# Kernel optimization log

Hardware: AMD Instinct MI355X
Metric: run time of the kernel (lower is better)

Reference implementation:

```python
import jax, jax.numpy as jnp
import numpy as np

H = 64  # hidden_size
B, T1, T2, T3 = 4096, 512, 256, 128


def setup_inputs() -> dict:
    key = jax.random.key(0)
    ks = jax.random.split(key, 18)
    s = 1.0 / np.sqrt(H)  # torch LSTMCell init scale
    def p(k, shape, scale):
        return jax.random.normal(k, shape, dtype=jnp.float32) * scale
    return {
        "x1": p(ks[0], (B, T1), 1.0),
        "x2": p(ks[1], (B, T2), 1.0),
        "x3": p(ks[2], (B, T3), 1.0),
        "W_ih3": p(ks[3], (4 * H, 3), s), "W_hh3": p(ks[4], (4 * H, H), s),
        "b_ih3": p(ks[5], (4 * H,), s), "b_hh3": p(ks[6], (4 * H,), s),
        "W_ih2": p(ks[7], (4 * H, 2), s), "W_hh2": p(ks[8], (4 * H, H), s),
        "b_ih2": p(ks[9], (4 * H,), s), "b_hh2": p(ks[10], (4 * H,), s),
        "W_ih1": p(ks[11], (4 * H, 1), s), "W_hh1": p(ks[12], (4 * H, H), s),
        "b_ih1": p(ks[13], (4 * H,), s), "b_hh1": p(ks[14], (4 * H,), s),
        "W_out": p(ks[15], (1, H), s), "b_out": p(ks[16], (1,), s),
    }


def reference(x1, x2, x3,
              W_ih3, W_hh3, b_ih3, b_hh3,
              W_ih2, W_hh2, b_ih2, b_hh2,
              W_ih1, W_hh1, b_ih1, b_hh1,
              W_out, b_out):
    h = W_hh3.shape[1]
    Bb, t1 = x1.shape
    r2, r3 = t1 // x2.shape[1], t1 // x3.shape[1]
    # Pad input weights to width 3; concat order is [x1, x2, x3] (zeros where absent),
    # so padded-column zeros reproduce the narrower cells exactly.
    Wi = jnp.stack([W_ih3,
                    jnp.pad(W_ih2, ((0, 0), (0, 1))),
                    jnp.pad(W_ih1, ((0, 0), (0, 2)))])  # [3, 4H, 3]
    Wh = jnp.stack([W_hh3, W_hh2, W_hh1])               # [3, 4H, H]
    bs = jnp.stack([b_ih3 + b_hh3, b_ih2 + b_hh2, b_ih1 + b_hh1])  # [3, 4H]
    t = np.arange(t1)
    has2 = (t % r2 == 0)
    has3 = (t % r3 == 0)
    assert not np.any(has3 & ~has2), "ratio2 must divide ratio3 for the concat-order mapping"
    # width 3 -> cell3 (type 0), width 2 -> cell2 (type 1), width 1 -> cell1 (type 2)
    step_type = jnp.asarray(2 - has2.astype(np.int32) - has3.astype(np.int32))
    xs = jnp.zeros((t1, Bb, 3), x1.dtype)
    xs = xs.at[:, :, 0].set(x1.T)
    xs = xs.at[::r2, :, 1].set(x2.T)
    xs = xs.at[::r3, :, 2].set(x3.T)

    def step(carry, inp):
        hx, cx = carry
        x, ty = inp
        g = x @ Wi[ty].T + hx @ Wh[ty].T + bs[ty]  # [B, 4H]
        i, f, gg, o = jnp.split(g, 4, axis=-1)     # torch gate order i,f,g,o
        cx = jax.nn.sigmoid(f) * cx + jax.nn.sigmoid(i) * jnp.tanh(gg)
        hx = jax.nn.sigmoid(o) * jnp.tanh(cx)
        return (hx, cx), None

    z = jnp.zeros((Bb, h), x1.dtype)
    (hx, _), _ = jax.lax.scan(step, (z, z), (xs, step_type))
    return jax.nn.sigmoid(hx @ W_out.T + b_out)  # [B, 1]
```

## Files before the change

### kernel.cpp

```cpp
#include <hip/hip_runtime.h>


typedef __attribute__((ext_vector_type(8))) short short8v;
typedef __attribute__((ext_vector_type(4))) float float4v;
typedef __attribute__((ext_vector_type(2))) float float2v;
typedef __attribute__((ext_vector_type(4))) unsigned int uint4v;
typedef __attribute__((ext_vector_type(2))) unsigned int uint2v;

template <int N> struct IC { static constexpr int value = N; };

#define AST 72
#define XSA 516
#define XSB 129

#if __has_builtin(__builtin_amdgcn_exp2f)
#define EXP2F(x) __builtin_amdgcn_exp2f(x)
#else
#define EXP2F(x) exp2f(x)
#endif
#if __has_builtin(__builtin_amdgcn_rcpf)
#define RCPF(x) __builtin_amdgcn_rcpf(x)
#else
#define RCPF(x) (1.0f / (x))
#endif

#define NL2E -1.4426950408889634f
#define NL2E2 -2.8853900817779268f

__device__ __forceinline__ short f2bf(float f) {
  union { float f; unsigned u; } v; v.f = f;
  unsigned r = v.u + 0x7FFFu + ((v.u >> 16) & 1u);
  return (short)(r >> 16);
}
__device__ __forceinline__ float bf2f(short h) {
  union { float f; unsigned u; } v;
  v.u = ((unsigned)(unsigned short)h) << 16;
  return v.f;
}
__device__ __forceinline__ unsigned cvt_pk_bf16(float lo, float hi) {
  unsigned r;
  asm("v_cvt_pk_bf16_f32 %0, %1, %2" : "=v"(r) : "v"(lo), "v"(hi));
  return r;
}
__device__ __forceinline__ float rcp1p(float y) {
  return RCPF(1.0f + EXP2F(y));
}
__device__ __forceinline__ float fsig(float x) { return rcp1p(x * NL2E); }

__global__ __launch_bounds__(256, 1) void mlstm_kernel(
    const float* __restrict__ x1, const float* __restrict__ x2,
    const float* __restrict__ x3,
    const float* __restrict__ Wi3, const float* __restrict__ Wh3,
    const float* __restrict__ bi3, const float* __restrict__ bh3,
    const float* __restrict__ Wi2, const float* __restrict__ Wh2,
    const float* __restrict__ bi2, const float* __restrict__ bh2,
    const float* __restrict__ Wi1, const float* __restrict__ Wh1,
    const float* __restrict__ bi1, const float* __restrict__ bh1,
    const float* __restrict__ Wout, const float* __restrict__ bout,
    float* __restrict__ out) {
  __shared__ __attribute__((aligned(16))) short Ab0[16 * AST];
  __shared__ __attribute__((aligned(16))) short Ab1[16 * AST];
  __shared__ __attribute__((aligned(16))) unsigned xAf[16 * XSA];
  __shared__ __attribute__((aligned(16))) unsigned xBf[16 * XSB];

  const int tid = threadIdx.x;
  const int w = tid >> 6;
  const int lane = tid & 63;
  const int q = lane >> 4;
  const int c = lane & 15;
  const int R0 = blockIdx.x << 4;

  for (int idx = tid; idx < 16 * 256; idx += 256) {
    int m = idx >> 8, tp = idx & 255;
    float2v v1 = *(const float2v*)(x1 + (size_t)(R0 + m) * 512 + 2 * tp);
    float v2 = x2[(size_t)(R0 + m) * 256 + tp];
    xAf[m * XSA + 2 * tp] = cvt_pk_bf16(v1[0], v2);
    xAf[m * XSA + 2 * tp + 1] = cvt_pk_bf16(v1[1], v2);
  }
  for (int idx = tid; idx < 16 * 128; idx += 256) {
    int m = idx >> 7, tt = idx & 127;
    xBf[m * XSB + tt] = cvt_pk_bf16(x3[(size_t)(R0 + m) * 128 + tt], 0.0f);
  }
  for (int idx = tid; idx < 16 * AST; idx += 256) {
    Ab0[idx] = 0;
    Ab1[idx] = 0;
  }

  short8v whs[3][4][2];
  short8v wix[3][4];
  float4v bias4[3][4];
  {
    const float* WhA[3] = {Wh3, Wh2, Wh1};
    const float* WiA[3] = {Wi3, Wi2, Wi1};
    const float* biA[3] = {bi3, bi2, bi1};
    const float* bhA[3] = {bh3, bh2, bh1};
    const int wdt[3] = {3, 2, 1};
#pragma unroll
    for (int ty = 0; ty < 3; ++ty) {
#pragma unroll
      for (int g = 0; g < 4; ++g) {
        const float sg = (g == 2) ? NL2E2 : NL2E;
        const int n = g * 64 + 16 * w + c;
#pragma unroll
        for (int kf = 0; kf < 2; ++kf) {
          short8v v;
#pragma unroll
          for (int j = 0; j < 8; ++j)
            v[j] = f2bf(sg * WhA[ty][n * 64 + kf * 32 + q * 8 + j]);
          whs[ty][g][kf] = v;
        }
        short8v v2 = {0, 0, 0, 0, 0, 0, 0, 0};
        if (q == 0) {
#pragma unroll
          for (int j = 0; j < 3; ++j)
            if (j < wdt[ty]) v2[j] = f2bf(sg * WiA[ty][n * wdt[ty] + j]);
        }
        wix[ty][g] = v2;
        float4v bv;
#pragma unroll
        for (int r = 0; r < 4; ++r) {
          const int nd = g * 64 + 16 * w + 4 * q + r;
          bv[r] = sg * (biA[ty][nd] + bhA[ty][nd]);
        }
        bias4[ty][g] = bv;
      }
    }
  }

  const int afo = c * AST + q * 8;
  const int hwo = c * AST + 16 * w + 4 * q;
  const int xao = c * XSA;
  const int xbo = c * XSB;

  __syncthreads();

  float cx[4] = {0.f, 0.f, 0.f, 0.f};

  auto stepf = [&](auto tyc, unsigned dS, unsigned dx3, const short* rbuf,
                   short* wbuf) {
    constexpr int TY = decltype(tyc)::value;
    uint4v au = {dS, dx3, 0u, 0u};
    short8v a2 = __builtin_bit_cast(short8v, au);
    short8v a0 = *(const short8v*)(rbuf + afo);
    short8v a1 = *(const short8v*)(rbuf + afo + 32);

    float4v acc[4];
#pragma unroll
    for (int g = 0; g < 4; ++g) {
      float4v z = bias4[TY][g];
      z = __builtin_amdgcn_mfma_f32_16x16x32_bf16(wix[TY][g], a2, z, 0, 0, 0);
      z = __builtin_amdgcn_mfma_f32_16x16x32_bf16(whs[TY][g][0], a0, z, 0, 0, 0);
      z = __builtin_amdgcn_mfma_f32_16x16x32_bf16(whs[TY][g][1], a1, z, 0, 0, 0);
      acc[g] = z;
    }

    float h[4];
#pragma unroll
    for (int r = 0; r < 4; ++r) {
      float e0 = EXP2F(acc[0][r]);
      float e1 = EXP2F(acc[1][r]);
      float e2 = EXP2F(__builtin_fminf(acc[2][r], 60.0f));
      float e3 = EXP2F(acc[3][r]);
      float a = 1.0f + e0, b = 1.0f + e1, g2 = 1.0f + e2;
      float ag = a * g2;
      float Rr = RCPF(ag * b);
      float ncx = (__builtin_fmaf(cx[r], ag, (1.0f - e2) * b)) * Rr;
      cx[r] = ncx;
      float e4 = EXP2F(__builtin_fminf(ncx * NL2E2, 60.0f));
      h[r] = (1.0f - e4) * RCPF((1.0f + e3) * (1.0f + e4));
    }
    uint2v pk;
    pk[0] = cvt_pk_bf16(h[0], h[1]);
    pk[1] = cvt_pk_bf16(h[2], h[3]);
    *(uint2v*)(wbuf + hwo) = pk;
    __syncthreads();
  };

  uint4v xd = *(const uint4v*)(xAf + xao);
  unsigned xw = xBf[xbo];

  for (int t4 = 0; t4 < 512; t4 += 4) {
    stepf(IC<0>{}, xd[0], xw, Ab0, Ab1);
    int tp = (t4 + 4 > 508) ? 508 : (t4 + 4);
    uint4v xdn = *(const uint4v*)(xAf + xao + tp);
    unsigned xwn = xBf[xbo + (tp >> 2)];
    stepf(IC<2>{}, xd[1], xw, Ab1, Ab0);
    stepf(IC<1>{}, xd[2], xw, Ab0, Ab1);
    stepf(IC<2>{}, xd[3], xw, Ab1, Ab0);
    xd = xdn;
    xw = xwn;
  }

  if (tid < 16) {
    float s = bout[0];
    const short* hr = Ab0 + tid * AST;
#pragma unroll
    for (int k = 0; k < 64; ++k)
      s = __builtin_fmaf(bf2f(hr[k]), Wout[k], s);
    out[R0 + tid] = fsig(s);
  }
}

extern "C" void kernel_launch(void* const* d_in, const int* in_sizes, int n_in,
                              void* d_out, int out_size, void* d_ws,
                              size_t ws_size, hipStream_t stream) {
  const float* x1 = (const float*)d_in[0];
  const float* x2 = (const float*)d_in[1];
  const float* x3 = (const float*)d_in[2];
  const float* Wi3 = (const float*)d_in[3];
  const float* Wh3 = (const float*)d_in[4];
  const float* bi3 = (const float*)d_in[5];
  const float* bh3 = (const float*)d_in[6];
  const float* Wi2 = (const float*)d_in[7];
  const float* Wh2 = (const float*)d_in[8];
  const float* bi2 = (const float*)d_in[9];
  const float* bh2 = (const float*)d_in[10];
  const float* Wi1 = (const float*)d_in[11];
  const float* Wh1 = (const float*)d_in[12];
  const float* bi1 = (const float*)d_in[13];
  const float* bh1 = (const float*)d_in[14];
  const float* Wout = (const float*)d_in[15];
  const float* bout = (const float*)d_in[16];
  float* out = (float*)d_out;

  hipLaunchKernelGGL(mlstm_kernel, dim3(256), dim3(256), 0, stream,
                     x1, x2, x3, Wi3, Wh3, bi3, bh3, Wi2, Wh2, bi2, bh2,
                     Wi1, Wh1, bi1, bh1, Wout, bout, out);
}
```

Before: 299.4 us.

## Split LSTM recurrence K-dimension across two wave groups with LDS partial-sum exchange

Doubles the block to 8 waves. Each pair of waves splits the hidden-state reduction into two K halves, trades partial gate sums through shared memory, and each finishes the nonlinearity for half the rows. This shortens the per-wave serial MFMA chain and halves per-wave elementwise work on the latency-bound recurrence. It adds a second block barrier and an LDS round-trip every timestep.

```diff
diff --git a/kernel.cpp b/kernel.cpp
--- a/kernel.cpp
+++ b/kernel.cpp
@@ -5,7 +5,6 @@
 typedef __attribute__((ext_vector_type(4))) float float4v;
 typedef __attribute__((ext_vector_type(2))) float float2v;
 typedef __attribute__((ext_vector_type(4))) unsigned int uint4v;
-typedef __attribute__((ext_vector_type(2))) unsigned int uint2v;
 
 template <int N> struct IC { static constexpr int value = N; };
 
@@ -47,7 +46,7 @@
 }
 __device__ __forceinline__ float fsig(float x) { return rcp1p(x * NL2E); }
 
-__global__ __launch_bounds__(256, 1) void mlstm_kernel(
+__global__ __launch_bounds__(512, 1) void mlstm_kernel(
     const float* __restrict__ x1, const float* __restrict__ x2,
     const float* __restrict__ x3,
     const float* __restrict__ Wi3, const float* __restrict__ Wh3,
@@ -62,31 +61,34 @@
   __shared__ __attribute__((aligned(16))) short Ab1[16 * AST];
   __shared__ __attribute__((aligned(16))) unsigned xAf[16 * XSA];
   __shared__ __attribute__((aligned(16))) unsigned xBf[16 * XSB];
+  __shared__ __attribute__((aligned(16))) float Pex[4][2][4][128];
 
   const int tid = threadIdx.x;
-  const int w = tid >> 6;
+  const int wv = tid >> 6;
+  const int p = wv & 3;
+  const int e = wv >> 2;
   const int lane = tid & 63;
   const int q = lane >> 4;
   const int c = lane & 15;
   const int R0 = blockIdx.x << 4;
 
-  for (int idx = tid; idx < 16 * 256; idx += 256) {
+  for (int idx = tid; idx < 16 * 256; idx += 512) {
     int m = idx >> 8, tp = idx & 255;
     float2v v1 = *(const float2v*)(x1 + (size_t)(R0 + m) * 512 + 2 * tp);
     float v2 = x2[(size_t)(R0 + m) * 256 + tp];
     xAf[m * XSA + 2 * tp] = cvt_pk_bf16(v1[0], v2);
     xAf[m * XSA + 2 * tp + 1] = cvt_pk_bf16(v1[1], v2);
   }
-  for (int idx = tid; idx < 16 * 128; idx += 256) {
+  for (int idx = tid; idx < 16 * 128; idx += 512) {
     int m = idx >> 7, tt = idx & 127;
     xBf[m * XSB + tt] = cvt_pk_bf16(x3[(size_t)(R0 + m) * 128 + tt], 0.0f);
   }
-  for (int idx = tid; idx < 16 * AST; idx += 256) {
+  for (int idx = tid; idx < 16 * AST; idx += 512) {
     Ab0[idx] = 0;
     Ab1[idx] = 0;
   }
 
-  short8v whs[3][4][2];
+  short8v whs[3][4];
   short8v wix[3][4];
   float4v bias4[3][4];
   {
@@ -100,17 +102,14 @@
 #pragma unroll
       for (int g = 0; g < 4; ++g) {
         const float sg = (g == 2) ? NL2E2 : NL2E;
-        const int n = g * 64 + 16 * w + c;
-#pragma unroll
-        for (int kf = 0; kf < 2; ++kf) {
-          short8v v;
-#pragma unroll
-          for (int j = 0; j < 8; ++j)
-            v[j] = f2bf(sg * WhA[ty][n * 64 + kf * 32 + q * 8 + j]);
-          whs[ty][g][kf] = v;
-        }
+        const int n = g * 64 + 16 * p + c;
+        short8v v;
+#pragma unroll
+        for (int j = 0; j < 8; ++j)
+          v[j] = f2bf(sg * WhA[ty][n * 64 + e * 32 + q * 8 + j]);
+        whs[ty][g] = v;
         short8v v2 = {0, 0, 0, 0, 0, 0, 0, 0};
-        if (q == 0) {
+        if (e == 0 && q == 0) {
 #pragma unroll
           for (int j = 0; j < 3; ++j)
             if (j < wdt[ty]) v2[j] = f2bf(sg * WiA[ty][n * wdt[ty] + j]);
@@ -119,7 +118,7 @@
         float4v bv;
 #pragma unroll
         for (int r = 0; r < 4; ++r) {
-          const int nd = g * 64 + 16 * w + 4 * q + r;
+          const int nd = g * 64 + 16 * p + 4 * q + r;
           bv[r] = sg * (biA[ty][nd] + bhA[ty][nd]);
         }
         bias4[ty][g] = bv;
@@ -127,63 +126,109 @@
     }
   }
 
-  const int afo = c * AST + q * 8;
-  const int hwo = c * AST + 16 * w + 4 * q;
+  const int afo = c * AST + q * 8 + e * 32;
+  const int hwo = c * AST + 16 * p + 4 * q + 2 * e;
+  float* pwr = &Pex[p][e][0][2 * lane];
+  const float* prd = &Pex[p][1 - e][0][2 * lane];
   const int xao = c * XSA;
   const int xbo = c * XSB;
 
   __syncthreads();
 
-  float cx[4] = {0.f, 0.f, 0.f, 0.f};
+  float cx0 = 0.f, cx1 = 0.f;
 
   auto stepf = [&](auto tyc, unsigned dS, unsigned dx3, const short* rbuf,
                    short* wbuf) {
     constexpr int TY = decltype(tyc)::value;
-    uint4v au = {dS, dx3, 0u, 0u};
-    short8v a2 = __builtin_bit_cast(short8v, au);
-    short8v a0 = *(const short8v*)(rbuf + afo);
-    short8v a1 = *(const short8v*)(rbuf + afo + 32);
+    short8v ah = *(const short8v*)(rbuf + afo);
 
     float4v acc[4];
-#pragma unroll
-    for (int g = 0; g < 4; ++g) {
-      float4v z = bias4[TY][g];
-      z = __builtin_amdgcn_mfma_f32_16x16x32_bf16(wix[TY][g], a2, z, 0, 0, 0);
-      z = __builtin_amdgcn_mfma_f32_16x16x32_bf16(whs[TY][g][0], a0, z, 0, 0, 0);
-      z = __builtin_amdgcn_mfma_f32_16x16x32_bf16(whs[TY][g][1], a1, z, 0, 0, 0);
-      acc[g] = z;
-    }
-
-    float h[4];
-#pragma unroll
-    for (int r = 0; r < 4; ++r) {
-      float e0 = EXP2F(acc[0][r]);
-      float e1 = EXP2F(acc[1][r]);
-      float e2 = EXP2F(__builtin_fminf(acc[2][r], 60.0f));
-      float e3 = EXP2F(acc[3][r]);
-      float a = 1.0f + e0, b = 1.0f + e1, g2 = 1.0f + e2;
+    if (e == 0) {
+      uint4v au = {dS, dx3, 0u, 0u};
+      short8v a2 = __builtin_bit_cast(short8v, au);
+#pragma unroll
+      for (int g = 0; g < 4; ++g) {
+        float4v z = bias4[TY][g];
+        z = __builtin_amdgcn_mfma_f32_16x16x32_bf16(wix[TY][g], a2, z, 0, 0, 0);
+        z = __builtin_amdgcn_mfma_f32_16x16x32_bf16(whs[TY][g], ah, z, 0, 0, 0);
+        acc[g] = z;
+      }
+    } else {
+      const float4v zz = {0.f, 0.f, 0.f, 0.f};
+#pragma unroll
+      for (int g = 0; g < 4; ++g)
+        acc[g] = __builtin_amdgcn_mfma_f32_16x16x32_bf16(whs[TY][g], ah, zz,
+                                                         0, 0, 0);
+    }
+
+    if (e == 0) {
+#pragma unroll
+      for (int g = 0; g < 4; ++g) {
+        float2v o = {acc[g][2], acc[g][3]};
+        *(float2v*)(pwr + g * 128) = o;
+      }
+    } else {
+#pragma unroll
+      for (int g = 0; g < 4; ++g) {
+        float2v o = {acc[g][0], acc[g][1]};
+        *(float2v*)(pwr + g * 128) = o;
+      }
+    }
+    __syncthreads();
+
+    float G[4][2];
+    if (e == 0) {
+#pragma unroll
+      for (int g = 0; g < 4; ++g) {
+        float2v pg = *(const float2v*)(prd + g * 128);
+        G[g][0] = acc[g][0] + pg[0];
+        G[g][1] = acc[g][1] + pg[1];
+      }
+    } else {
+#pragma unroll
+      for (int g = 0; g < 4; ++g) {
+        float2v pg = *(const float2v*)(prd + g * 128);
+        G[g][0] = acc[g][2] + pg[0];
+        G[g][1] = acc[g][3] + pg[1];
+      }
+    }
+
+    float h2[2];
+#pragma unroll
+    for (int u = 0; u < 2; ++u) {
+      float e0v = EXP2F(G[0][u]);
+      float e1v = EXP2F(G[1][u]);
+      float e2v = EXP2F(__builtin_fminf(G[2][u], 60.0f));
+      float e3v = EXP2F(G[3][u]);
+      float a = 1.0f + e0v, b = 1.0f + e1v, g2 = 1.0f + e2v;
       float ag = a * g2;
       float Rr = RCPF(ag * b);
-      float ncx = (__builtin_fmaf(cx[r], ag, (1.0f - e2) * b)) * Rr;
-      cx[r] = ncx;
-      float e4 = EXP2F(__builtin_fminf(ncx * NL2E2, 60.0f));
-      h[r] = (1.0f - e4) * RCPF((1.0f + e3) * (1.0f + e4));
-    }
-    uint2v pk;
-    pk[0] = cvt_pk_bf16(h[0], h[1]);
-    pk[1] = cvt_pk_bf16(h[2], h[3]);
-    *(uint2v*)(wbuf + hwo) = pk;
+      float cxu = u ? cx1 : cx0;
+      float ncx = __builtin_fmaf(cxu, ag, (1.0f - e2v) * b) * Rr;
+      if (u) cx1 = ncx; else cx0 = ncx;
+      float e4v = EXP2F(__builtin_fminf(ncx * NL2E2, 60.0f));
+      h2[u] = (1.0f - e4v) * RCPF((1.0f + e3v) * (1.0f + e4v));
+    }
+    *(unsigned*)(wbuf + hwo) = cvt_pk_bf16(h2[0], h2[1]);
     __syncthreads();
   };
 
-  uint4v xd = *(const uint4v*)(xAf + xao);
-  unsigned xw = xBf[xbo];
+  uint4v xd = {0u, 0u, 0u, 0u};
+  unsigned xw = 0u;
+  if (e == 0) {
+    xd = *(const uint4v*)(xAf + xao);
+    xw = xBf[xbo];
+  }
 
   for (int t4 = 0; t4 < 512; t4 += 4) {
     stepf(IC<0>{}, xd[0], xw, Ab0, Ab1);
-    int tp = (t4 + 4 > 508) ? 508 : (t4 + 4);
-    uint4v xdn = *(const uint4v*)(xAf + xao + tp);
-    unsigned xwn = xBf[xbo + (tp >> 2)];
+    uint4v xdn = xd;
+    unsigned xwn = xw;
+    if (e == 0) {
+      int tp = (t4 + 4 > 508) ? 508 : (t4 + 4);
+      xdn = *(const uint4v*)(xAf + xao + tp);
+      xwn = xBf[xbo + (tp >> 2)];
+    }
     stepf(IC<2>{}, xd[1], xw, Ab1, Ab0);
     stepf(IC<1>{}, xd[2], xw, Ab0, Ab1);
     stepf(IC<2>{}, xd[3], xw, Ab1, Ab0);
@@ -223,7 +268,7 @@
   const float* bout = (const float*)d_in[16];
   float* out = (float*)d_out;
 
-  hipLaunchKernelGGL(mlstm_kernel, dim3(256), dim3(256), 0, stream,
+  hipLaunchKernelGGL(mlstm_kernel, dim3(256), dim3(512), 0, stream,
                      x1, x2, x3, Wi3, Wh3, bi3, bh3, Wi2, Wh2, bi2, bh2,
                      Wi1, Wh1, bi1, bh1, Wout, bout, out);
 }
```

Measured after the change: 421.9 us. 40.9% more time.

## Precompute next step's input-projection MFMA off the critical path; pair reciprocals

Applied to the files above, without the earlier changes.

Moves the x@Wi+bias MFMA for step t+1 into step t, issued after the recurrent MFMAs, so each step's serial chain has two dependent MFMAs instead of three. The activation math now handles two rows at a time and shares one reciprocal between them (two products instead of two RCPs), which cuts the number of transcendental ops. The exp clamps are lowered to 30 and 36 so the paired products stay finite. In exchange it keeps an extra set of accumulator registers live and adds a few multiplies.

```diff
diff --git a/kernel.cpp b/kernel.cpp
--- a/kernel.cpp
+++ b/kernel.cpp
@@ -136,42 +136,62 @@
 
   float cx[4] = {0.f, 0.f, 0.f, 0.f};
 
-  auto stepf = [&](auto tyc, unsigned dS, unsigned dx3, const short* rbuf,
-                   short* wbuf) {
+  float4v zxA[4], zxB[4];
+
+  auto stepf = [&](auto tyc, auto tync, unsigned dSn, unsigned dx3n,
+                   const short* rbuf, short* wbuf, float4v (&zin)[4],
+                   float4v (&zout)[4]) {
     constexpr int TY = decltype(tyc)::value;
-    uint4v au = {dS, dx3, 0u, 0u};
-    short8v a2 = __builtin_bit_cast(short8v, au);
+    constexpr int TYN = decltype(tync)::value;
     short8v a0 = *(const short8v*)(rbuf + afo);
     short8v a1 = *(const short8v*)(rbuf + afo + 32);
 
     float4v acc[4];
 #pragma unroll
     for (int g = 0; g < 4; ++g) {
-      float4v z = bias4[TY][g];
-      z = __builtin_amdgcn_mfma_f32_16x16x32_bf16(wix[TY][g], a2, z, 0, 0, 0);
-      z = __builtin_amdgcn_mfma_f32_16x16x32_bf16(whs[TY][g][0], a0, z, 0, 0, 0);
-      z = __builtin_amdgcn_mfma_f32_16x16x32_bf16(whs[TY][g][1], a1, z, 0, 0, 0);
-      acc[g] = z;
+      float4v z =
+          __builtin_amdgcn_mfma_f32_16x16x32_bf16(whs[TY][g][0], a0, zin[g], 0, 0, 0);
+      acc[g] =
+          __builtin_amdgcn_mfma_f32_16x16x32_bf16(whs[TY][g][1], a1, z, 0, 0, 0);
     }
 
-    float h[4];
-#pragma unroll
-    for (int r = 0; r < 4; ++r) {
-      float e0 = EXP2F(acc[0][r]);
-      float e1 = EXP2F(acc[1][r]);
-      float e2 = EXP2F(__builtin_fminf(acc[2][r], 60.0f));
-      float e3 = EXP2F(acc[3][r]);
-      float a = 1.0f + e0, b = 1.0f + e1, g2 = 1.0f + e2;
-      float ag = a * g2;
-      float Rr = RCPF(ag * b);
-      float ncx = (__builtin_fmaf(cx[r], ag, (1.0f - e2) * b)) * Rr;
-      cx[r] = ncx;
-      float e4 = EXP2F(__builtin_fminf(ncx * NL2E2, 60.0f));
-      h[r] = (1.0f - e4) * RCPF((1.0f + e3) * (1.0f + e4));
+    uint4v aun = {dSn, dx3n, 0u, 0u};
+    short8v a2n = __builtin_bit_cast(short8v, aun);
+#pragma unroll
+    for (int g = 0; g < 4; ++g)
+      zout[g] = __builtin_amdgcn_mfma_f32_16x16x32_bf16(wix[TYN][g], a2n,
+                                                        bias4[TYN][g], 0, 0, 0);
+
+    float h4[4];
+#pragma unroll
+    for (int pr = 0; pr < 2; ++pr) {
+      const int r0 = 2 * pr, r1 = 2 * pr + 1;
+      float e0a = EXP2F(acc[0][r0]), e0b = EXP2F(acc[0][r1]);
+      float e1a = EXP2F(acc[1][r0]), e1b = EXP2F(acc[1][r1]);
+      float e2a = EXP2F(__builtin_fminf(acc[2][r0], 30.0f));
+      float e2b = EXP2F(__builtin_fminf(acc[2][r1], 30.0f));
+      float aa = 1.0f + e0a, ba = 1.0f + e1a, ga = 1.0f + e2a;
+      float ab_ = 1.0f + e0b, bb = 1.0f + e1b, gb = 1.0f + e2b;
+      float aga = aa * ga, agb = ab_ * gb;
+      float Da = aga * ba, Db = agb * bb;
+      float Rp = RCPF(Da * Db);
+      float Ra = Rp * Db, Rb = Rp * Da;
+      float nca = __builtin_fmaf(cx[r0], aga, (1.0f - e2a) * ba) * Ra;
+      float ncb = __builtin_fmaf(cx[r1], agb, (1.0f - e2b) * bb) * Rb;
+      cx[r0] = nca;
+      cx[r1] = ncb;
+      float e3a = EXP2F(acc[3][r0]), e3b = EXP2F(acc[3][r1]);
+      float e4a = EXP2F(__builtin_fminf(nca * NL2E2, 36.0f));
+      float e4b = EXP2F(__builtin_fminf(ncb * NL2E2, 36.0f));
+      float D2a = (1.0f + e3a) * (1.0f + e4a);
+      float D2b = (1.0f + e3b) * (1.0f + e4b);
+      float R2 = RCPF(D2a * D2b);
+      h4[r0] = (1.0f - e4a) * (R2 * D2b);
+      h4[r1] = (1.0f - e4b) * (R2 * D2a);
     }
     uint2v pk;
-    pk[0] = cvt_pk_bf16(h[0], h[1]);
-    pk[1] = cvt_pk_bf16(h[2], h[3]);
+    pk[0] = cvt_pk_bf16(h4[0], h4[1]);
+    pk[1] = cvt_pk_bf16(h4[2], h4[3]);
     *(uint2v*)(wbuf + hwo) = pk;
     __syncthreads();
   };
@@ -179,14 +199,23 @@
   uint4v xd = *(const uint4v*)(xAf + xao);
   unsigned xw = xBf[xbo];
 
+  {
+    uint4v au = {xd[0], xw, 0u, 0u};
+    short8v a2 = __builtin_bit_cast(short8v, au);
+#pragma unroll
+    for (int g = 0; g < 4; ++g)
+      zxA[g] = __builtin_amdgcn_mfma_f32_16x16x32_bf16(wix[0][g], a2,
+                                                       bias4[0][g], 0, 0, 0);
+  }
+
   for (int t4 = 0; t4 < 512; t4 += 4) {
-    stepf(IC<0>{}, xd[0], xw, Ab0, Ab1);
+    stepf(IC<0>{}, IC<2>{}, xd[1], xw, Ab0, Ab1, zxA, zxB);
     int tp = (t4 + 4 > 508) ? 508 : (t4 + 4);
     uint4v xdn = *(const uint4v*)(xAf + xao + tp);
     unsigned xwn = xBf[xbo + (tp >> 2)];
-    stepf(IC<2>{}, xd[1], xw, Ab1, Ab0);
-    stepf(IC<1>{}, xd[2], xw, Ab0, Ab1);
-    stepf(IC<2>{}, xd[3], xw, Ab1, Ab0);
+    stepf(IC<2>{}, IC<1>{}, xd[2], xw, Ab1, Ab0, zxB, zxA);
+    stepf(IC<1>{}, IC<2>{}, xd[3], xw, Ab0, Ab1, zxA, zxB);
+    stepf(IC<2>{}, IC<0>{}, xdn[0], xwn, Ab1, Ab0, zxB, zxA);
     xd = xdn;
     xw = xwn;
   }
```

After: 306.3 us. 1.02x slower.

## Duplicate MFMA per wave pair and split gate activations across 512 threads

Applied to the files above, without the earlier changes.

Doubles the block to 512 threads. Each pair of waves computes the same MFMA gate products redundantly, and each wave then evaluates the activations for only half of the four accumulator rows. Bias is added after the MFMA instead of being seeded into the accumulator. The aim is to halve the serial transcendental work per step on the recurrent critical path. In exchange it doubles MFMA issue, makes the per-step barrier cover 8 waves, adds register pressure under launch_bounds(512,2), and introduces a divergent e==0 branch.

```diff
diff --git a/kernel.cpp b/kernel.cpp
--- a/kernel.cpp
+++ b/kernel.cpp
@@ -5,7 +5,6 @@
 typedef __attribute__((ext_vector_type(4))) float float4v;
 typedef __attribute__((ext_vector_type(2))) float float2v;
 typedef __attribute__((ext_vector_type(4))) unsigned int uint4v;
-typedef __attribute__((ext_vector_type(2))) unsigned int uint2v;
 
 template <int N> struct IC { static constexpr int value = N; };
 
@@ -47,7 +46,7 @@
 }
 __device__ __forceinline__ float fsig(float x) { return rcp1p(x * NL2E); }
 
-__global__ __launch_bounds__(256, 1) void mlstm_kernel(
+__global__ __launch_bounds__(512, 2) void mlstm_kernel(
     const float* __restrict__ x1, const float* __restrict__ x2,
     const float* __restrict__ x3,
     const float* __restrict__ Wi3, const float* __restrict__ Wh3,
@@ -64,31 +63,32 @@
   __shared__ __attribute__((aligned(16))) unsigned xBf[16 * XSB];
 
   const int tid = threadIdx.x;
-  const int w = tid >> 6;
+  const int w = (tid >> 6) & 3;
+  const int e = tid >> 8;
   const int lane = tid & 63;
   const int q = lane >> 4;
   const int c = lane & 15;
   const int R0 = blockIdx.x << 4;
 
-  for (int idx = tid; idx < 16 * 256; idx += 256) {
+  for (int idx = tid; idx < 16 * 256; idx += 512) {
     int m = idx >> 8, tp = idx & 255;
     float2v v1 = *(const float2v*)(x1 + (size_t)(R0 + m) * 512 + 2 * tp);
     float v2 = x2[(size_t)(R0 + m) * 256 + tp];
     xAf[m * XSA + 2 * tp] = cvt_pk_bf16(v1[0], v2);
     xAf[m * XSA + 2 * tp + 1] = cvt_pk_bf16(v1[1], v2);
   }
-  for (int idx = tid; idx < 16 * 128; idx += 256) {
+  for (int idx = tid; idx < 16 * 128; idx += 512) {
     int m = idx >> 7, tt = idx & 127;
     xBf[m * XSB + tt] = cvt_pk_bf16(x3[(size_t)(R0 + m) * 128 + tt], 0.0f);
   }
-  for (int idx = tid; idx < 16 * AST; idx += 256) {
+  for (int idx = tid; idx < 16 * AST; idx += 512) {
     Ab0[idx] = 0;
     Ab1[idx] = 0;
   }
 
   short8v whs[3][4][2];
   short8v wix[3][4];
-  float4v bias4[3][4];
+  float2v bias2[3][4];
   {
     const float* WhA[3] = {Wh3, Wh2, Wh1};
     const float* WiA[3] = {Wi3, Wi2, Wi1};
@@ -116,25 +116,26 @@
             if (j < wdt[ty]) v2[j] = f2bf(sg * WiA[ty][n * wdt[ty] + j]);
         }
         wix[ty][g] = v2;
-        float4v bv;
-#pragma unroll
-        for (int r = 0; r < 4; ++r) {
-          const int nd = g * 64 + 16 * w + 4 * q + r;
-          bv[r] = sg * (biA[ty][nd] + bhA[ty][nd]);
+        float2v bv;
+#pragma unroll
+        for (int u = 0; u < 2; ++u) {
+          const int nd = g * 64 + 16 * w + 4 * q + 2 * e + u;
+          bv[u] = sg * (biA[ty][nd] + bhA[ty][nd]);
         }
-        bias4[ty][g] = bv;
+        bias2[ty][g] = bv;
       }
     }
   }
 
   const int afo = c * AST + q * 8;
-  const int hwo = c * AST + 16 * w + 4 * q;
+  const int hwo = c * AST + 16 * w + 4 * q + 2 * e;
   const int xao = c * XSA;
   const int xbo = c * XSB;
 
   __syncthreads();
 
-  float cx[4] = {0.f, 0.f, 0.f, 0.f};
+  float cx2[2] = {0.f, 0.f};
+  const float4v ZZ = {0.f, 0.f, 0.f, 0.f};
 
   auto stepf = [&](auto tyc, unsigned dS, unsigned dx3, const short* rbuf,
                    short* wbuf) {
@@ -147,32 +148,36 @@
     float4v acc[4];
 #pragma unroll
     for (int g = 0; g < 4; ++g) {
-      float4v z = bias4[TY][g];
-      z = __builtin_amdgcn_mfma_f32_16x16x32_bf16(wix[TY][g], a2, z, 0, 0, 0);
+      float4v z = __builtin_amdgcn_mfma_f32_16x16x32_bf16(wix[TY][g], a2, ZZ, 0, 0, 0);
       z = __builtin_amdgcn_mfma_f32_16x16x32_bf16(whs[TY][g][0], a0, z, 0, 0, 0);
-      z = __builtin_amdgcn_mfma_f32_16x16x32_bf16(whs[TY][g][1], a1, z, 0, 0, 0);
-      acc[g] = z;
+      acc[g] = __builtin_amdgcn_mfma_f32_16x16x32_bf16(whs[TY][g][1], a1, z, 0, 0, 0);
     }
 
-    float h[4];
-#pragma unroll
-    for (int r = 0; r < 4; ++r) {
-      float e0 = EXP2F(acc[0][r]);
-      float e1 = EXP2F(acc[1][r]);
-      float e2 = EXP2F(__builtin_fminf(acc[2][r], 60.0f));
-      float e3 = EXP2F(acc[3][r]);
-      float a = 1.0f + e0, b = 1.0f + e1, g2 = 1.0f + e2;
-      float ag = a * g2;
-      float Rr = RCPF(ag * b);
-      float ncx = (__builtin_fmaf(cx[r], ag, (1.0f - e2) * b)) * Rr;
-      cx[r] = ncx;
-      float e4 = EXP2F(__builtin_fminf(ncx * NL2E2, 60.0f));
-      h[r] = (1.0f - e4) * RCPF((1.0f + e3) * (1.0f + e4));
-    }
-    uint2v pk;
-    pk[0] = cvt_pk_bf16(h[0], h[1]);
-    pk[1] = cvt_pk_bf16(h[2], h[3]);
-    *(uint2v*)(wbuf + hwo) = pk;
+    auto act2 = [&](auto baseC) {
+      constexpr int B0 = decltype(baseC)::value;
+      float h2[2];
+#pragma unroll
+      for (int u = 0; u < 2; ++u) {
+        float G0 = acc[0][B0 + u] + bias2[TY][0][u];
+        float G1 = acc[1][B0 + u] + bias2[TY][1][u];
+        float G2 = acc[2][B0 + u] + bias2[TY][2][u];
+        float G3 = acc[3][B0 + u] + bias2[TY][3][u];
+        float e0 = EXP2F(G0);
+        float e1 = EXP2F(G1);
+        float e2 = EXP2F(__builtin_fminf(G2, 60.0f));
+        float e3 = EXP2F(G3);
+        float a = 1.0f + e0, b = 1.0f + e1, g2 = 1.0f + e2;
+        float ag = a * g2;
+        float Rr = RCPF(ag * b);
+        float ncx = __builtin_fmaf(cx2[u], ag, (1.0f - e2) * b) * Rr;
+        cx2[u] = ncx;
+        float e4 = EXP2F(__builtin_fminf(ncx * NL2E2, 60.0f));
+        h2[u] = (1.0f - e4) * RCPF((1.0f + e3) * (1.0f + e4));
+      }
+      *(unsigned*)(wbuf + hwo) = cvt_pk_bf16(h2[0], h2[1]);
+    };
+    if (e == 0) act2(IC<0>{});
+    else       act2(IC<2>{});
     __syncthreads();
   };
 
@@ -223,7 +228,7 @@
   const float* bout = (const float*)d_in[16];
   float* out = (float*)d_out;
 
-  hipLaunchKernelGGL(mlstm_kernel, dim3(256), dim3(256), 0, stream,
+  hipLaunchKernelGGL(mlstm_kernel, dim3(256), dim3(512), 0, stream,
                      x1, x2, x3, Wi3, Wh3, bi3, bh3, Wi2, Wh2, bi2, bh2,
                      Wi1, Wh1, bi1, bh1, Wout, bout, out);
 }
```

New measurement: 332.6 us. 1.11x slower.
